# Performance work log

Hardware: AMD Instinct MI355X
Metric: run time of the kernel (lower is better)

The kernel has to match this reference:

```python
import jax, jax.numpy as jnp
import numpy as np

K = 27  # num_neighs, hardcoded in module
EPS = 1e-5


def knn_idx(x, k):
    # x: (B, N, 3) -> (B, N, k) indices of k nearest neighbors (self included)
    xx = jnp.sum(x * x, axis=-1)                      # (B, N)
    inner = jnp.einsum('bnd,bmd->bnm', x, x)          # (B, N, N)
    d = 2.0 * inner - xx[:, :, None] - xx[:, None, :] # negative sq dist
    return jax.lax.top_k(d, k)[1]


def graph_feature(f, idx):
    # f: (B, N, C), idx: (B, N, k) -> (B, N, k, 2C) = [neigh - center, center]
    neigh = jax.vmap(lambda fb, ib: fb[ib])(f, idx)   # (B, N, k, C)
    center = jnp.broadcast_to(f[:, :, None, :], neigh.shape)
    return jnp.concatenate([neigh - center, center], axis=-1)


def bn_lrelu(y, g, b, axes):
    m = jnp.mean(y, axis=axes, keepdims=True)
    v = jnp.var(y, axis=axes, keepdims=True)
    y = (y - m) * jax.lax.rsqrt(v + EPS) * g + b
    return jnp.where(y >= 0, y, 0.2 * y)


def edge_conv(f, idx, W, g, b):
    # f: (B, N, C) -> (B, N, C_out); 1x1 conv over (B, 2C, N, k) + BN + LeakyReLU + max over k
    h = graph_feature(f, idx)                         # (B, N, k, 2C)
    y = jnp.einsum('bnkc,oc->bnko', h, W)             # (B, N, k, C_out)
    y = bn_lrelu(y, g, b, axes=(0, 1, 2))
    return jnp.max(y, axis=2)                         # (B, N, C_out)


def setup_inputs() -> dict:
    key = jax.random.key(0)
    ks = jax.random.split(key, 8)
    B, N, latent = 2, 2048, 256
    x = jax.random.normal(ks[0], (B, N, 3), dtype=jnp.float32)
    chans = [(6, 96), (192, 192), (384, 384), (768, 768)]
    inp = {'x': x}
    for i, (cin, cout) in enumerate(chans):
        inp[f'W{i}'] = jax.random.normal(ks[1 + i], (cout, cin), dtype=jnp.float32) * np.sqrt(2.0 / cin).astype(np.float32)
        inp[f'g{i}'] = jnp.ones((cout,), dtype=jnp.float32)
        inp[f'b{i}'] = jnp.zeros((cout,), dtype=jnp.float32)
    inp['W4'] = jax.random.normal(ks[5], (latent, 1440), dtype=jnp.float32) * np.sqrt(2.0 / 1440).astype(np.float32)
    inp['g4'] = jnp.ones((latent,), dtype=jnp.float32)
    inp['b4'] = jnp.zeros((latent,), dtype=jnp.float32)
    return inp


def reference(x, W0, g0, b0, W1, g1, b1, W2, g2, b2, W3, g3, b3, W4, g4, b4):
    # x: (B, N, 3)
    idx = knn_idx(x, K)                               # (B, N, K), fixed for all layers (only_true_neighs=True)
    outs = []
    f = x
    for (W, g, b) in ((W0, g0, b0), (W1, g1, b1), (W2, g2, b2), (W3, g3, b3)):
        f = edge_conv(f, idx, W, g, b)
        outs.append(f)
    h = jnp.concatenate(outs, axis=-1)                # (B, N, 1440)
    y = jnp.einsum('bnc,oc->bno', h, W4)              # (B, N, latent)
    feats = bn_lrelu(y, g4, b4, axes=(0, 1))          # features_per_point (B, N, latent)
    global_feat = jnp.max(feats, axis=1)              # (B, latent)
    return global_feat, feats
```

## Files before the change

### kernel.cpp

```cpp
#include <hip/hip_runtime.h>
#include <hip/hip_bf16.h>

#define BATCH 2
#define NPB   2048
#define NPTS  4096
#define KNB   27
#define FCATC 1440
#define CSTRIDE 1696
#define NSLOT 32
#define PBATCH 4

#define WOFF_L1 0
#define WOFF_L2 36864
#define WOFF_L3 184320
#define WOFF_F  774144
#define WTOTAL  1142784

typedef __hip_bfloat16 bf16;
typedef __attribute__((ext_vector_type(8))) short short8;
typedef __attribute__((ext_vector_type(4))) float f32x4;
typedef __attribute__((ext_vector_type(2))) short s16x2;

__device__ __forceinline__ float b2f(bf16 v) { return __bfloat162float(v); }

__device__ __forceinline__ void split_bf16(float v, bf16& h, bf16& l) {
    h = __float2bfloat16(v);
    l = __float2bfloat16(v - b2f(h));
}

__device__ __forceinline__ float ldin(const void* p, size_t i, int f32) {
    return f32 ? ((const float*)p)[i] : b2f(((const bf16*)p)[i]);
}

__device__ __forceinline__ void gl16(const bf16* g, bf16* l) {
    __builtin_amdgcn_global_load_lds(
        (const __attribute__((address_space(1))) unsigned int*)g,
        (__attribute__((address_space(3))) unsigned int*)l,
        16, 0, 0);
}

__global__ void k_init(const void* __restrict__ x, int* __restrict__ flag,
                       float* __restrict__ xf, float* __restrict__ slots) {
    if (blockIdx.x < 424) {
        slots[blockIdx.x * 256 + threadIdx.x] = 0.f;
        return;
    }
    __shared__ int s;
    if (threadIdx.x == 0) s = 0;
    __syncthreads();
    const bf16* xb = (const bf16*)x;
    int local = 0;
    for (int i = threadIdx.x; i < NPTS * 3; i += 256) {
        float v = b2f(xb[i]);
        if (!(fabsf(v) < 1e4f)) local = 1;
    }
    if (local) s = 1;
    __syncthreads();
    int f32 = s;
    if (threadIdx.x == 0) flag[0] = f32;
    for (int i = threadIdx.x; i < NPTS * 3; i += 256) xf[i] = ldin(x, i, f32);
}

__global__ __launch_bounds__(256) void k_knn(const float* __restrict__ x, int* __restrict__ idx) {
    __shared__ uint hist4[4][260];
    __shared__ uint hist[256];
    __shared__ uint tkey[NPB];
    __shared__ int  tix[NPB];
    __shared__ uint s_phigh;
    __shared__ int  s_rem, s_outcnt, s_tiecnt;

    int bn = blockIdx.x, b = bn >> 11, n = bn & (NPB - 1);
    int tid = threadIdx.x;
    int wv = tid >> 6;
    const float* xb = x + (size_t)b * NPB * 3;
    float cx = xb[n * 3 + 0], cy = xb[n * 3 + 1], cz = xb[n * 3 + 2];
    float cc = cx * cx + cy * cy + cz * cz;

    uint u[8];
    #pragma unroll
    for (int j = 0; j < 8; j++) {
        int m = j * 256 + tid;
        float mx = xb[m * 3 + 0], my = xb[m * 3 + 1], mz = xb[m * 3 + 2];
        float d = 2.f * (cx * mx + cy * my + cz * mz) - cc - (mx * mx + my * my + mz * mz);
        uint s = __float_as_uint(d);
        u[j] = (s & 0x80000000u) ? ~s : (s | 0x80000000u);
    }
    if (tid == 0) { s_phigh = 0; s_rem = KNB; s_outcnt = 0; s_tiecnt = 0; }

    for (int pass = 0; pass < 2; pass++) {
        int shift = 24 - pass * 8;
        hist[tid] = 0;
        for (int i = tid; i < 4 * 260; i += 256) ((uint*)hist4)[i] = 0;
        __syncthreads();
        uint phigh = s_phigh;
        #pragma unroll
        for (int j = 0; j < 8; j++) {
            bool in = (pass == 0) || ((u[j] >> (shift + 8)) == phigh);
            if (in) atomicAdd(&hist4[wv][(u[j] >> shift) & 0xFFu], 1u);
        }
        __syncthreads();
        hist[tid] = hist4[0][tid] + hist4[1][tid] + hist4[2][tid] + hist4[3][tid];
        __syncthreads();
        if (tid < 64) {
            int L = tid;
            uint c0 = hist[L * 4 + 0], c1 = hist[L * 4 + 1], c2 = hist[L * 4 + 2], c3 = hist[L * 4 + 3];
            uint s = c0 + c1 + c2 + c3;
            uint acc = s;
            #pragma unroll
            for (int off = 1; off < 64; off <<= 1) {
                uint t = __shfl_down(acc, off);
                if (L + off < 64) acc += t;
            }
            uint excl = acc - s;
            int rem = s_rem;
            if ((int)excl < rem && (int)acc >= rem) {
                uint cs[4] = { c0, c1, c2, c3 };
                uint cum = excl;
                int bsel = 0; uint hb = 0;
                #pragma unroll
                for (int q = 3; q >= 0; q--) {
                    if ((int)cum < rem && (int)(cum + cs[q]) >= rem && hb == 0u && bsel == 0) {
                        bsel = L * 4 + q; hb = cs[q]; cum += cs[q];
                    } else if (bsel == 0 && hb == 0u) {
                        cum += cs[q];
                    }
                }
                int strictlyAbove = (int)(cum - hb);
                s_rem = rem - strictlyAbove;
                s_phigh = (phigh << 8) | (uint)bsel;
            }
        }
        __syncthreads();
    }

    uint T16 = s_phigh;
    #pragma unroll
    for (int j = 0; j < 8; j++) {
        int m = j * 256 + tid;
        uint hi = u[j] >> 16;
        if (hi > T16) {
            int p = atomicAdd(&s_outcnt, 1);
            idx[bn * KNB + p] = b * NPB + m;
        } else if (hi == T16) {
            int p = atomicAdd(&s_tiecnt, 1);
            tkey[p] = u[j];
            tix[p] = m;
        }
    }
    __syncthreads();
    int outcnt = s_outcnt, rem = s_rem, tiecnt = s_tiecnt;
    if (tiecnt == rem) {
        if (tid < rem) idx[bn * KNB + outcnt + tid] = b * NPB + tix[tid];
    } else if (tid == 0) {
        for (int t = 0; t < rem; t++) {
            int bi = 0;
            for (int q = 1; q < tiecnt; q++)
                if (tkey[q] > tkey[bi] || (tkey[q] == tkey[bi] && tix[q] < tix[bi])) bi = q;
            idx[bn * KNB + outcnt + t] = b * NPB + tix[bi];
            tkey[bi] = 0; tix[bi] = 0x7fffffff;
        }
    }
}

__global__ void k_l0(const float* __restrict__ xf, const void* __restrict__ W,
                     const int* __restrict__ flag, bf16* __restrict__ Ub, float* __restrict__ Vf) {
    int i = blockIdx.x * 256 + threadIdx.x;
    if (i >= NPTS * 192) return;
    int bn = i / 192, o = i % 192;
    int f32 = flag[0];
    float x0 = xf[bn * 3 + 0], x1 = xf[bn * 3 + 1], x2 = xf[bn * 3 + 2];
    if (o < 96) {
        float r = x0 * ldin(W, o * 6 + 0, f32) + x1 * ldin(W, o * 6 + 1, f32) + x2 * ldin(W, o * 6 + 2, f32);
        Ub[(size_t)bn * 96 + o] = __float2bfloat16(r);
    } else {
        int oo = o - 96;
        float w0 = ldin(W, oo * 6 + 3, f32) - ldin(W, oo * 6 + 0, f32);
        float w1 = ldin(W, oo * 6 + 4, f32) - ldin(W, oo * 6 + 1, f32);
        float w2 = ldin(W, oo * 6 + 5, f32) - ldin(W, oo * 6 + 2, f32);
        Vf[(size_t)bn * 96 + oo] = x0 * w0 + x1 * w1 + x2 * w2;
    }
}

__global__ void k_wt_all(const void* __restrict__ W1, const void* __restrict__ W2,
                         const void* __restrict__ W3, const void* __restrict__ W4,
                         const int* __restrict__ flag,
                         bf16* __restrict__ Wh, bf16* __restrict__ Wl) {
    int i = blockIdx.x * 256 + threadIdx.x;
    if (i >= WTOTAL) return;
    int f32 = flag[0];
    float w;
    if (i < WOFF_L2) {
        int row = i / 96, c = i % 96;
        w = (row < 192) ? ldin(W1, (size_t)row * 192 + c, f32)
                        : ldin(W1, (size_t)(row - 192) * 192 + 96 + c, f32)
                          - ldin(W1, (size_t)(row - 192) * 192 + c, f32);
    } else if (i < WOFF_L3) {
        int j = i - WOFF_L2;
        int row = j / 192, c = j % 192;
        w = (row < 384) ? ldin(W2, (size_t)row * 384 + c, f32)
                        : ldin(W2, (size_t)(row - 384) * 384 + 192 + c, f32)
                          - ldin(W2, (size_t)(row - 384) * 384 + c, f32);
    } else if (i < WOFF_F) {
        int j = i - WOFF_L3;
        int row = j / 384, c = j % 384;
        w = (row < 768) ? ldin(W3, (size_t)row * 768 + c, f32)
                        : ldin(W3, (size_t)(row - 768) * 768 + 384 + c, f32)
                          - ldin(W3, (size_t)(row - 768) * 768 + c, f32);
    } else {
        int j = i - WOFF_F;
        w = ldin(W4, j, f32);
    }
    bf16 h, l; split_bf16(w, h, l);
    Wh[i] = h; Wl[i] = l;
}

template<int TM, int TN>
__global__ __launch_bounds__(256) void k_gemm_mfma(const bf16* __restrict__ Ah, const bf16* __restrict__ Al,
                                                   int lda, int aoff,
                                                   const bf16* __restrict__ Bh, const bf16* __restrict__ Bl,
                                                   int K, bf16* __restrict__ Cu, float* __restrict__ Cv,
                                                   int Cosplit, int ldc, int ksz, int zstride) {
    constexpr int FRM  = TM / 32;
    constexpr int FRN  = TN / 32;
    constexpr int ISSA = TM / 64;
    constexpr int ISSB = TN / 64;
    constexpr int MY   = (NPTS / TM) / 8;
    __shared__ __align__(16) bf16 Ash[2][TM][32];
    __shared__ __align__(16) bf16 Asl[2][TM][32];
    __shared__ __align__(16) bf16 Bsh[2][TN][32];
    __shared__ __align__(16) bf16 Bsl[2][TN][32];
    int tid = threadIdx.x;
    int wave = tid >> 6, lane = tid & 63;
    int wm = wave >> 1, wn = wave & 1;
    int quad = lane >> 4, l15 = lane & 15;
    int Lxy = blockIdx.y * gridDim.x + blockIdx.x;
    int stripe = Lxy & 7;
    int w = Lxy >> 3;
    int mb = stripe * MY + (w & (MY - 1));
    int nb = w / MY;
    int m0 = mb * TM, n0 = nb * TN;
    int kbase = blockIdx.z * ksz;
    float* Cz = Cv + (size_t)blockIdx.z * zstride;

    int ra_s[ISSA], ca_s[ISSA];
    #pragma unroll
    for (int i = 0; i < ISSA; i++) {
        int c = wave * 64 + lane + i * 256;
        ra_s[i] = c >> 2;
        ca_s[i] = (((c & 3) ^ ((c >> 3) & 3)) << 3);
    }
    int rb_s[ISSB], cb_s[ISSB];
    #pragma unroll
    for (int i = 0; i < ISSB; i++) {
        int c = wave * 64 + lane + i * 256;
        rb_s[i] = c >> 2;
        cb_s[i] = (((c & 3) ^ ((c >> 3) & 3)) << 3);
    }

    auto STAGE = [&](int buf, int k0) {
        #pragma unroll
        for (int i = 0; i < ISSA; i++) {
            size_t ga = (size_t)(m0 + ra_s[i]) * lda + aoff + k0 + ca_s[i];
            gl16(Ah + ga, &Ash[buf][0][0] + wave * 512 + i * 2048);
            gl16(Al + ga, &Asl[buf][0][0] + wave * 512 + i * 2048);
        }
        #pragma unroll
        for (int i = 0; i < ISSB; i++) {
            size_t gb = (size_t)(n0 + rb_s[i]) * K + k0 + cb_s[i];
            gl16(Bh + gb, &Bsh[buf][0][0] + wave * 512 + i * 2048);
            gl16(Bl + gb, &Bsl[buf][0][0] + wave * 512 + i * 2048);
        }
    };

    int nsteps = ksz >> 5;
    f32x4 acc[FRM][FRN] = {};
    STAGE(0, kbase);
    __syncthreads();
    int cur = 0;
    for (int t = 0; t < nsteps; t++) {
        if (t + 1 < nsteps) STAGE(cur ^ 1, kbase + ((t + 1) << 5));
        short8 ahf[FRM], alf[FRM], bhf[FRN], blf[FRN];
        #pragma unroll
        for (int mt = 0; mt < FRM; mt++) {
            int rr = wm * (TM / 2) + mt * 16 + l15;
            int qs = (quad ^ ((rr >> 1) & 3)) * 8;
            ahf[mt] = *(const short8*)&Ash[cur][rr][qs];
            alf[mt] = *(const short8*)&Asl[cur][rr][qs];
        }
        #pragma unroll
        for (int nt = 0; nt < FRN; nt++) {
            int rr = wn * (TN / 2) + nt * 16 + l15;
            int qs = (quad ^ ((rr >> 1) & 3)) * 8;
            bhf[nt] = *(const short8*)&Bsh[cur][rr][qs];
            blf[nt] = *(const short8*)&Bsl[cur][rr][qs];
        }
        #pragma unroll
        for (int mt = 0; mt < FRM; mt++) {
            #pragma unroll
            for (int nt = 0; nt < FRN; nt++) {
                acc[mt][nt] = __builtin_amdgcn_mfma_f32_16x16x32_bf16(ahf[mt], blf[nt], acc[mt][nt], 0, 0, 0);
                acc[mt][nt] = __builtin_amdgcn_mfma_f32_16x16x32_bf16(alf[mt], bhf[nt], acc[mt][nt], 0, 0, 0);
                acc[mt][nt] = __builtin_amdgcn_mfma_f32_16x16x32_bf16(ahf[mt], bhf[nt], acc[mt][nt], 0, 0, 0);
            }
        }
        __syncthreads();
        cur ^= 1;
    }
    #pragma unroll
    for (int mt = 0; mt < FRM; mt++) {
        #pragma unroll
        for (int nt = 0; nt < FRN; nt++) {
            int col = n0 + wn * (TN / 2) + nt * 16 + l15;
            #pragma unroll
            for (int i = 0; i < 4; i++) {
                int row = m0 + wm * (TM / 2) + mt * 16 + quad * 4 + i;
                if (Cosplit > 0) {
                    if (col < Cosplit) Cu[(size_t)row * Cosplit + col] = __float2bfloat16(acc[mt][nt][i]);
                    else               Cv[(size_t)row * Cosplit + col - Cosplit] = acc[mt][nt][i];
                } else {
                    Cz[(size_t)row * ldc + col] = acc[mt][nt][i];
                }
            }
        }
    }
}

__global__ __launch_bounds__(256) void k_gather(const bf16* __restrict__ Ub, float* __restrict__ Vf,
                                                const int* __restrict__ idx,
                                                bf16* __restrict__ fch, bf16* __restrict__ fcl,
                                                float* __restrict__ ssum, float* __restrict__ ssq,
                                                int Co, int out_off) {
    __shared__ int srow[PBATCH * KNB];
    int tid = threadIdx.x;
    int L = blockIdx.y * gridDim.x + blockIdx.x;
    int batch = L & 1;
    int w = L >> 1;
    int pg = batch * 512 + (w & 511);
    int chunk = w >> 9;
    int p0 = pg * PBATCH;
    if (tid < PBATCH * KNB) srow[tid] = idx[p0 * KNB + tid] * Co;
    __syncthreads();
    int P = Co >> 1;
    int op = chunk * 256 + tid;
    if (op >= P) return;
    int o = op * 2;
    int slot = pg & (NSLOT - 1);
    float s0 = 0.f, s1 = 0.f, q0 = 0.f, q1 = 0.f;
    #pragma unroll 1
    for (int p = 0; p < PBATCH; p++) {
        int bn = p0 + p;
        float2 vv = *(const float2*)&Vf[(size_t)bn * Co + o];
        float ymax0 = -INFINITY, ymax1 = -INFINITY, ymin0 = INFINITY, ymin1 = INFINITY;
        #pragma unroll
        for (int k = 0; k < KNB; k++) {
            uint wb = *(const uint*)&Ub[(size_t)srow[p * KNB + k] + o];
            float y0 = __uint_as_float(wb << 16) + vv.x;
            float y1 = __uint_as_float(wb & 0xffff0000u) + vv.y;
            ymax0 = fmaxf(ymax0, y0); ymin0 = fminf(ymin0, y0); s0 += y0; q0 += y0 * y0;
            ymax1 = fmaxf(ymax1, y1); ymin1 = fminf(ymin1, y1); s1 += y1; q1 += y1 * y1;
        }
        size_t fi = (size_t)bn * FCATC + out_off + o;
        bf16 hh[2], ll[2];
        split_bf16(ymax0, hh[0], ll[0]);
        split_bf16(ymax1, hh[1], ll[1]);
        *(s16x2*)&fch[fi] = *(const s16x2*)hh;
        *(s16x2*)&fcl[fi] = *(const s16x2*)ll;
        *(float2*)&Vf[(size_t)bn * Co + o] = make_float2(ymin0, ymin1);
    }
    atomicAdd(&ssum[slot * CSTRIDE + o + 0], s0);
    atomicAdd(&ssum[slot * CSTRIDE + o + 1], s1);
    atomicAdd(&ssq [slot * CSTRIDE + o + 0], q0);
    atomicAdd(&ssq [slot * CSTRIDE + o + 1], q1);
}

__global__ void k_scaleshift(const float* __restrict__ ssum, const float* __restrict__ ssq,
                             const void* __restrict__ g, const void* __restrict__ bb,
                             const int* __restrict__ flag,
                             float* __restrict__ scale, float* __restrict__ shift, int Co, float invcnt) {
    int o = blockIdx.x * 256 + threadIdx.x;
    if (o >= Co) return;
    int f32 = flag[0];
    float s = 0.f, q = 0.f;
    for (int c = 0; c < NSLOT; c++) { s += ssum[c * CSTRIDE + o]; q += ssq[c * CSTRIDE + o]; }
    float mean = s * invcnt;
    float var = q * invcnt - mean * mean;
    float sc = ldin(g, o, f32) * rsqrtf(var + 1e-5f);
    scale[o] = sc;
    shift[o] = ldin(bb, o, f32) - mean * sc;
}

__global__ __launch_bounds__(256) void k_apply(const float* __restrict__ Vf,
                                               const float* __restrict__ scale, const float* __restrict__ shift,
                                               bf16* __restrict__ fch, bf16* __restrict__ fcl,
                                               int Co, int out_off) {
    int bn = blockIdx.x;
    for (int o = threadIdx.x; o < Co; o += 256) {
        float sc = scale[o], sh = shift[o];
        size_t fi = (size_t)bn * FCATC + out_off + o;
        float y = (sc >= 0.f) ? (b2f(fch[fi]) + b2f(fcl[fi]))
                              : Vf[(size_t)bn * Co + o];
        float z = sc * y + sh;
        z = (z >= 0.f) ? z : 0.2f * z;
        bf16 h, l; split_bf16(z, h, l);
        fch[fi] = h; fcl[fi] = l;
    }
}

__global__ void k_stats_final(const float* __restrict__ part, float* __restrict__ Y,
                              float* __restrict__ ssum, float* __restrict__ ssq) {
    int o = threadIdx.x;
    int p0 = blockIdx.x * 16;
    int slot = blockIdx.x & (NSLOT - 1);
    const size_t PL = (size_t)NPTS * 256;
    float s = 0, q = 0;
    for (int p = 0; p < 16; p++) {
        size_t i = (size_t)(p0 + p) * 256 + o;
        float y = part[i] + part[i + PL] + part[i + 2 * PL] + part[i + 3 * PL] + part[i + 4 * PL];
        Y[i] = y;
        s += y; q += y * y;
    }
    atomicAdd(&ssum[slot * CSTRIDE + o], s);
    atomicAdd(&ssq [slot * CSTRIDE + o], q);
}

__global__ void k_feats(const float* __restrict__ Y, const float* __restrict__ ssum,
                        const float* __restrict__ ssq, const void* __restrict__ g,
                        const void* __restrict__ bb, const int* __restrict__ flag,
                        void* __restrict__ out, float* __restrict__ partial) {
    int o = threadIdx.x;
    int chunk = blockIdx.x;
    int bn0 = chunk * 32;
    int f32 = flag[0];
    float s = 0.f, q = 0.f;
    for (int c = 0; c < NSLOT; c++) { s += ssum[c * CSTRIDE + o]; q += ssq[c * CSTRIDE + o]; }
    float mean = s * (1.f / (float)NPTS);
    float var = q * (1.f / (float)NPTS) - mean * mean;
    float sc = ldin(g, o, f32) * rsqrtf(var + 1e-5f);
    float sh = ldin(bb, o, f32) - mean * sc;
    float best = -INFINITY;
    for (int i = 0; i < 32; i++) {
        int bn = bn0 + i;
        float z = sc * Y[(size_t)bn * 256 + o] + sh;
        z = (z >= 0.f) ? z : 0.2f * z;
        size_t oi = (size_t)BATCH * 256 + (size_t)bn * 256 + o;
        if (f32) ((float*)out)[oi] = z;
        else     ((bf16*)out)[oi] = __float2bfloat16(z);
        best = fmaxf(best, z);
    }
    partial[chunk * 256 + o] = best;
}

__global__ void k_gmax(const float* __restrict__ partial, void* __restrict__ out, const int* __restrict__ flag) {
    int o = threadIdx.x;
    int b = blockIdx.x;
    float best = -INFINITY;
    for (int c = 0; c < 64; c++) best = fmaxf(best, partial[(b * 64 + c) * 256 + o]);
    if (flag[0]) ((float*)out)[b * 256 + o] = best;
    else         ((bf16*)out)[b * 256 + o] = __float2bfloat16(best);
}

extern "C" void kernel_launch(void* const* d_in, const int* in_sizes, int n_in,
                              void* d_out, int out_size, void* d_ws, size_t ws_size,
                              hipStream_t stream) {
    const void* x = d_in[0];

    char* ws = (char*)d_ws;
    int*   idx    = (int*)  (ws + 0);
    bf16*  Ub     = (bf16*) (ws + 442368);
    float* Vf     = (float*)(ws + 6733824);
    float* part   = (float*)(ws + 442368);
    bf16*  fch    = (bf16*) (ws + 25608192);
    bf16*  fcl    = (bf16*) (ws + 37404672);
    float* Y4     = (float*)(ws + 49201152);
    bf16*  Whall  = (bf16*) (ws + 53395456);
    bf16*  Wlall  = (bf16*) (ws + 55681024);
    float* slots  = (float*)(ws + 57966592);
    float* ssum   = slots;
    float* ssq    = slots + NSLOT * CSTRIDE;
    float* scales = (float*)(ws + 58400768);
    float* shifts = (float*)(ws + 58407552);
    float* partial= (float*)(ws + 442368);
    float* xf     = (float*)(ws + 58479872);
    int*   flag   = (int*)  (ws + 58529024);

    const int Cin[4]  = {3, 96, 192, 384};
    const int Co[4]   = {96, 192, 384, 768};
    const int ooff[4] = {0, 96, 288, 672};
    const int soff[5] = {0, 96, 288, 672, 1440};
    const int woff[4] = {0, WOFF_L1, WOFF_L2, WOFF_L3};

    hipLaunchKernelGGL(k_init, dim3(425), dim3(256), 0, stream, x, flag, xf, slots);
    hipLaunchKernelGGL(k_knn, dim3(NPTS), dim3(256), 0, stream, xf, idx);
    hipLaunchKernelGGL(k_wt_all, dim3((WTOTAL + 255) / 256), dim3(256), 0, stream,
                       d_in[4], d_in[7], d_in[10], d_in[13], flag, Whall, Wlall);

    const float invcnt_edge = 1.f / (float)(NPTS * KNB);
    for (int L = 0; L < 4; L++) {
        const void* g  = d_in[2 + 3 * L];
        const void* bb = d_in[3 + 3 * L];
        int N2 = 2 * Co[L];
        if (L == 0) {
            hipLaunchKernelGGL(k_l0, dim3((NPTS * 192 + 255) / 256), dim3(256), 0, stream,
                               xf, d_in[1], flag, Ub, Vf);
        } else if (L < 3) {
            hipLaunchKernelGGL((k_gemm_mfma<64, 64>), dim3(N2 / 64, NPTS / 64, 1), dim3(256), 0, stream,
                               fch, fcl, FCATC, ooff[L - 1], Whall + woff[L], Wlall + woff[L], Cin[L],
                               Ub, Vf, Co[L], 0, Cin[L], 0);
        } else {
            hipLaunchKernelGGL((k_gemm_mfma<128, 64>), dim3(N2 / 64, NPTS / 128, 1), dim3(256), 0, stream,
                               fch, fcl, FCATC, ooff[L - 1], Whall + woff[L], Wlall + woff[L], Cin[L],
                               Ub, Vf, Co[L], 0, Cin[L], 0);
        }
        int nchunks = ((Co[L] / 2) + 255) / 256;
        hipLaunchKernelGGL(k_gather, dim3(NPTS / PBATCH, nchunks), dim3(256), 0, stream,
                           Ub, Vf, idx, fch, fcl, ssum + soff[L], ssq + soff[L], Co[L], ooff[L]);
        hipLaunchKernelGGL(k_scaleshift, dim3((Co[L] + 255) / 256), dim3(256), 0, stream,
                           ssum + soff[L], ssq + soff[L], g, bb, flag,
                           scales + soff[L], shifts + soff[L], Co[L], invcnt_edge);
        hipLaunchKernelGGL(k_apply, dim3(NPTS), dim3(256), 0, stream,
                           Vf, scales + soff[L], shifts + soff[L], fch, fcl, Co[L], ooff[L]);
    }

    hipLaunchKernelGGL((k_gemm_mfma<128, 64>), dim3(256 / 64, NPTS / 128, 5), dim3(256), 0, stream,
                       fch, fcl, FCATC, 0, Whall + WOFF_F, Wlall + WOFF_F, FCATC,
                       (bf16*)nullptr, part, 0, 256, 288, NPTS * 256);
    hipLaunchKernelGGL(k_stats_final, dim3(256), dim3(256), 0, stream, part, Y4, ssum + soff[4], ssq + soff[4]);
    hipLaunchKernelGGL(k_feats, dim3(128), dim3(256), 0, stream, Y4, ssum + soff[4], ssq + soff[4],
                       d_in[14], d_in[15], flag, d_out, partial);
    hipLaunchKernelGGL(k_gmax, dim3(BATCH), dim3(256), 0, stream, partial, d_out, flag);
}
```

Measured before the change: 320.1 us.

## Fuse BN scale/shift and global max into producer kernels via last-block counters

```diff
diff --git a/kernel.cpp b/kernel.cpp
--- a/kernel.cpp
+++ b/kernel.cpp
@@ -40,11 +40,14 @@
 }
 
 __global__ void k_init(const void* __restrict__ x, int* __restrict__ flag,
-                       float* __restrict__ xf, float* __restrict__ slots) {
+                       float* __restrict__ xf, float* __restrict__ slots,
+                       int* __restrict__ cnt, int* __restrict__ enc) {
     if (blockIdx.x < 424) {
         slots[blockIdx.x * 256 + threadIdx.x] = 0.f;
         return;
     }
+    if (threadIdx.x < 8) cnt[threadIdx.x] = 0;
+    for (int i = threadIdx.x; i < 512; i += 256) enc[i] = 0;
     __shared__ int s;
     if (threadIdx.x == 0) s = 0;
     __syncthreads();
@@ -329,64 +332,70 @@
                                                 const int* __restrict__ idx,
                                                 bf16* __restrict__ fch, bf16* __restrict__ fcl,
                                                 float* __restrict__ ssum, float* __restrict__ ssq,
-                                                int Co, int out_off) {
+                                                int Co, int out_off,
+                                                const void* __restrict__ g, const void* __restrict__ bb,
+                                                const int* __restrict__ flag,
+                                                float* __restrict__ scale, float* __restrict__ shift,
+                                                float invcnt, int* __restrict__ cnt, int total) {
     __shared__ int srow[PBATCH * KNB];
+    __shared__ int s_last;
     int tid = threadIdx.x;
     int L = blockIdx.y * gridDim.x + blockIdx.x;
-    int batch = L & 1;
-    int w = L >> 1;
-    int pg = batch * 512 + (w & 511);
-    int chunk = w >> 9;
+    int batch = (L >> 2) & 1;
+    int pg = batch * 512 + (L & 3) * 128 + ((L >> 3) & 127);
+    int chunk = L >> 10;
     int p0 = pg * PBATCH;
     if (tid < PBATCH * KNB) srow[tid] = idx[p0 * KNB + tid] * Co;
     __syncthreads();
     int P = Co >> 1;
     int op = chunk * 256 + tid;
-    if (op >= P) return;
-    int o = op * 2;
-    int slot = pg & (NSLOT - 1);
-    float s0 = 0.f, s1 = 0.f, q0 = 0.f, q1 = 0.f;
-    #pragma unroll 1
-    for (int p = 0; p < PBATCH; p++) {
-        int bn = p0 + p;
-        float2 vv = *(const float2*)&Vf[(size_t)bn * Co + o];
-        float ymax0 = -INFINITY, ymax1 = -INFINITY, ymin0 = INFINITY, ymin1 = INFINITY;
-        #pragma unroll
-        for (int k = 0; k < KNB; k++) {
-            uint wb = *(const uint*)&Ub[(size_t)srow[p * KNB + k] + o];
-            float y0 = __uint_as_float(wb << 16) + vv.x;
-            float y1 = __uint_as_float(wb & 0xffff0000u) + vv.y;
-            ymax0 = fmaxf(ymax0, y0); ymin0 = fminf(ymin0, y0); s0 += y0; q0 += y0 * y0;
-            ymax1 = fmaxf(ymax1, y1); ymin1 = fminf(ymin1, y1); s1 += y1; q1 += y1 * y1;
-        }
-        size_t fi = (size_t)bn * FCATC + out_off + o;
-        bf16 hh[2], ll[2];
-        split_bf16(ymax0, hh[0], ll[0]);
-        split_bf16(ymax1, hh[1], ll[1]);
-        *(s16x2*)&fch[fi] = *(const s16x2*)hh;
-        *(s16x2*)&fcl[fi] = *(const s16x2*)ll;
-        *(float2*)&Vf[(size_t)bn * Co + o] = make_float2(ymin0, ymin1);
-    }
-    atomicAdd(&ssum[slot * CSTRIDE + o + 0], s0);
-    atomicAdd(&ssum[slot * CSTRIDE + o + 1], s1);
-    atomicAdd(&ssq [slot * CSTRIDE + o + 0], q0);
-    atomicAdd(&ssq [slot * CSTRIDE + o + 1], q1);
-}
-
-__global__ void k_scaleshift(const float* __restrict__ ssum, const float* __restrict__ ssq,
-                             const void* __restrict__ g, const void* __restrict__ bb,
-                             const int* __restrict__ flag,
-                             float* __restrict__ scale, float* __restrict__ shift, int Co, float invcnt) {
-    int o = blockIdx.x * 256 + threadIdx.x;
-    if (o >= Co) return;
-    int f32 = flag[0];
-    float s = 0.f, q = 0.f;
-    for (int c = 0; c < NSLOT; c++) { s += ssum[c * CSTRIDE + o]; q += ssq[c * CSTRIDE + o]; }
-    float mean = s * invcnt;
-    float var = q * invcnt - mean * mean;
-    float sc = ldin(g, o, f32) * rsqrtf(var + 1e-5f);
-    scale[o] = sc;
-    shift[o] = ldin(bb, o, f32) - mean * sc;
+    if (op < P) {
+        int o = op * 2;
+        int slot = pg & (NSLOT - 1);
+        float s0 = 0.f, s1 = 0.f, q0 = 0.f, q1 = 0.f;
+        #pragma unroll 1
+        for (int p = 0; p < PBATCH; p++) {
+            int bn = p0 + p;
+            float2 vv = *(const float2*)&Vf[(size_t)bn * Co + o];
+            float ymax0 = -INFINITY, ymax1 = -INFINITY, ymin0 = INFINITY, ymin1 = INFINITY;
+            #pragma unroll
+            for (int k = 0; k < KNB; k++) {
+                uint wb = *(const uint*)&Ub[(size_t)srow[p * KNB + k] + o];
+                float y0 = __uint_as_float(wb << 16) + vv.x;
+                float y1 = __uint_as_float(wb & 0xffff0000u) + vv.y;
+                ymax0 = fmaxf(ymax0, y0); ymin0 = fminf(ymin0, y0); s0 += y0; q0 += y0 * y0;
+                ymax1 = fmaxf(ymax1, y1); ymin1 = fminf(ymin1, y1); s1 += y1; q1 += y1 * y1;
+            }
+            size_t fi = (size_t)bn * FCATC + out_off + o;
+            bf16 hh[2], ll[2];
+            split_bf16(ymax0, hh[0], ll[0]);
+            split_bf16(ymax1, hh[1], ll[1]);
+            *(s16x2*)&fch[fi] = *(const s16x2*)hh;
+            *(s16x2*)&fcl[fi] = *(const s16x2*)ll;
+            *(float2*)&Vf[(size_t)bn * Co + o] = make_float2(ymin0, ymin1);
+        }
+        atomicAdd(&ssum[slot * CSTRIDE + o + 0], s0);
+        atomicAdd(&ssum[slot * CSTRIDE + o + 1], s1);
+        atomicAdd(&ssq [slot * CSTRIDE + o + 0], q0);
+        atomicAdd(&ssq [slot * CSTRIDE + o + 1], q1);
+    }
+    __threadfence();
+    __syncthreads();
+    if (tid == 0) s_last = (atomicAdd(cnt, 1) == total - 1);
+    __syncthreads();
+    if (s_last) {
+        __threadfence();
+        int f32 = flag[0];
+        for (int o = tid; o < Co; o += 256) {
+            float s = 0.f, q = 0.f;
+            for (int c = 0; c < NSLOT; c++) { s += ssum[c * CSTRIDE + o]; q += ssq[c * CSTRIDE + o]; }
+            float mean = s * invcnt;
+            float var = q * invcnt - mean * mean;
+            float sc = ldin(g, o, f32) * rsqrtf(var + 1e-5f);
+            scale[o] = sc;
+            shift[o] = ldin(bb, o, f32) - mean * sc;
+        }
+    }
 }
 
 __global__ __launch_bounds__(256) void k_apply(const float* __restrict__ Vf,
@@ -426,7 +435,8 @@
 __global__ void k_feats(const float* __restrict__ Y, const float* __restrict__ ssum,
                         const float* __restrict__ ssq, const void* __restrict__ g,
                         const void* __restrict__ bb, const int* __restrict__ flag,
-                        void* __restrict__ out, float* __restrict__ partial) {
+                        void* __restrict__ out, int* __restrict__ enc, int* __restrict__ cnt) {
+    __shared__ int s_last;
     int o = threadIdx.x;
     int chunk = blockIdx.x;
     int bn0 = chunk * 32;
@@ -447,16 +457,23 @@
         else     ((bf16*)out)[oi] = __float2bfloat16(z);
         best = fmaxf(best, z);
     }
-    partial[chunk * 256 + o] = best;
-}
-
-__global__ void k_gmax(const float* __restrict__ partial, void* __restrict__ out, const int* __restrict__ flag) {
-    int o = threadIdx.x;
-    int b = blockIdx.x;
-    float best = -INFINITY;
-    for (int c = 0; c < 64; c++) best = fmaxf(best, partial[(b * 64 + c) * 256 + o]);
-    if (flag[0]) ((float*)out)[b * 256 + o] = best;
-    else         ((bf16*)out)[b * 256 + o] = __float2bfloat16(best);
+    uint ub = __float_as_uint(best);
+    uint key = (ub & 0x80000000u) ? ~ub : (ub | 0x80000000u);
+    int b = chunk >> 6;
+    atomicMax((unsigned int*)&enc[b * 256 + o], key);
+    __threadfence();
+    if (o == 0) s_last = (atomicAdd(cnt, 1) == 127);
+    __syncthreads();
+    if (s_last) {
+        __threadfence();
+        for (int i = o; i < 512; i += 256) {
+            uint k2 = ((const uint*)enc)[i];
+            uint u2 = (k2 & 0x80000000u) ? (k2 & 0x7fffffffu) : ~k2;
+            float v = __uint_as_float(u2);
+            if (f32) ((float*)out)[i] = v;
+            else     ((bf16*)out)[i] = __float2bfloat16(v);
+        }
+    }
 }
 
 extern "C" void kernel_launch(void* const* d_in, const int* in_sizes, int n_in,
@@ -479,9 +496,10 @@
     float* ssq    = slots + NSLOT * CSTRIDE;
     float* scales = (float*)(ws + 58400768);
     float* shifts = (float*)(ws + 58407552);
-    float* partial= (float*)(ws + 442368);
     float* xf     = (float*)(ws + 58479872);
     int*   flag   = (int*)  (ws + 58529024);
+    int*   cnt    = (int*)  (ws + 58529280);
+    int*   enc    = (int*)  (ws + 58529536);
 
     const int Cin[4]  = {3, 96, 192, 384};
     const int Co[4]   = {96, 192, 384, 768};
@@ -489,7 +507,7 @@
     const int soff[5] = {0, 96, 288, 672, 1440};
     const int woff[4] = {0, WOFF_L1, WOFF_L2, WOFF_L3};
 
-    hipLaunchKernelGGL(k_init, dim3(425), dim3(256), 0, stream, x, flag, xf, slots);
+    hipLaunchKernelGGL(k_init, dim3(425), dim3(256), 0, stream, x, flag, xf, slots, cnt, enc);
     hipLaunchKernelGGL(k_knn, dim3(NPTS), dim3(256), 0, stream, xf, idx);
     hipLaunchKernelGGL(k_wt_all, dim3((WTOTAL + 255) / 256), dim3(256), 0, stream,
                        d_in[4], d_in[7], d_in[10], d_in[13], flag, Whall, Wlall);
@@ -513,10 +531,9 @@
         }
         int nchunks = ((Co[L] / 2) + 255) / 256;
         hipLaunchKernelGGL(k_gather, dim3(NPTS / PBATCH, nchunks), dim3(256), 0, stream,
-                           Ub, Vf, idx, fch, fcl, ssum + soff[L], ssq + soff[L], Co[L], ooff[L]);
-        hipLaunchKernelGGL(k_scaleshift, dim3((Co[L] + 255) / 256), dim3(256), 0, stream,
-                           ssum + soff[L], ssq + soff[L], g, bb, flag,
-                           scales + soff[L], shifts + soff[L], Co[L], invcnt_edge);
+                           Ub, Vf, idx, fch, fcl, ssum + soff[L], ssq + soff[L], Co[L], ooff[L],
+                           g, bb, flag, scales + soff[L], shifts + soff[L], invcnt_edge,
+                           cnt + L, (NPTS / PBATCH) * nchunks);
         hipLaunchKernelGGL(k_apply, dim3(NPTS), dim3(256), 0, stream,
                            Vf, scales + soff[L], shifts + soff[L], fch, fcl, Co[L], ooff[L]);
     }
@@ -526,6 +543,5 @@
                        (bf16*)nullptr, part, 0, 256, 288, NPTS * 256);
     hipLaunchKernelGGL(k_stats_final, dim3(256), dim3(256), 0, stream, part, Y4, ssum + soff[4], ssq + soff[4]);
     hipLaunchKernelGGL(k_feats, dim3(128), dim3(256), 0, stream, Y4, ssum + soff[4], ssq + soff[4],
-                       d_in[14], d_in[15], flag, d_out, partial);
-    hipLaunchKernelGGL(k_gmax, dim3(BATCH), dim3(256), 0, stream, partial, d_out, flag);
-}
+                       d_in[14], d_in[15], flag, d_out, enc, cnt + 4);
+}
```

After: 741.3 us. +131.6%, slower.
